# Optimization experiments

Measured on AMD Instinct MI355X. Metric: run time of the kernel, lower is better.

## Reference

```python
import jax, jax.numpy as jnp
import numpy as np

N = 50000      # nodes
E = 800000     # edges
F = 128        # node feature dim (= output_size, residual)
H = 128        # hidden_size

def _uniform_fan_avg(key, shape):
    # VarianceScaling(scale=1.0, mode='fan_avg', distribution='uniform')
    fan_avg = (shape[0] + shape[1]) / 2.0
    limit = np.sqrt(3.0 / fan_avg)
    return jax.random.uniform(key, shape, jnp.float32, -limit, limit)

def setup_inputs() -> dict:
    key = jax.random.key(0)
    ks = jax.random.split(key, 16)
    h = jax.random.normal(ks[0], (N, F), jnp.float32)
    pos = jax.random.normal(ks[1], (N, 3), jnp.float32)
    senders = jax.random.randint(ks[2], (E,), 0, N, jnp.int32)
    receivers = jax.random.randint(ks[3], (E,), 0, N, jnp.int32)
    # edge_mlp: Linear(2F+1 -> H) silu, Linear(H -> H) silu (activate_final=True)
    eW1 = _uniform_fan_avg(ks[4], (2 * F + 1, H)); eb1 = jnp.zeros((H,), jnp.float32)
    eW2 = _uniform_fan_avg(ks[5], (H, H)); eb2 = jnp.zeros((H,), jnp.float32)
    # node_mlp: Linear(F+H -> H) silu, Linear(H -> F) (no final act)
    nW1 = _uniform_fan_avg(ks[6], (F + H, H)); nb1 = jnp.zeros((H,), jnp.float32)
    nW2 = _uniform_fan_avg(ks[7], (H, F)); nb2 = jnp.zeros((F,), jnp.float32)
    # pos_correction_mlp: Linear(H -> H) silu, Linear(H -> 1, no bias, UniformScaling(dt))
    pW1 = _uniform_fan_avg(ks[8], (H, H)); pb1 = jnp.zeros((H,), jnp.float32)
    dt = 0.001
    pW2 = jax.random.uniform(ks[9], (H, 1), jnp.float32, -dt, dt) * np.sqrt(3.0)
    return {"h": h, "pos": pos, "senders": senders, "receivers": receivers,
            "eW1": eW1, "eb1": eb1, "eW2": eW2, "eb2": eb2,
            "nW1": nW1, "nb1": nb1, "nW2": nW2, "nb2": nb2,
            "pW1": pW1, "pb1": pb1, "pW2": pW2}

def reference(h, pos, senders, receivers,
              eW1, eb1, eW2, eb2,
              nW1, nb1, nW2, nb2,
              pW1, pb1, pW2):
    n = h.shape[0]
    # _coord2radial (normalize=False)
    coord_diff = pos[senders] - pos[receivers]            # [E,3]
    radial = jnp.sum(coord_diff ** 2, axis=1, keepdims=True)  # [E,1]
    # edge update (_message): concat(h[senders], h[receivers], radial) -> edge_mlp
    msg_in = jnp.concatenate([h[senders], h[receivers], radial], axis=-1)  # [E,2F+1]
    msg = jax.nn.silu(msg_in @ eW1 + eb1)
    msg = jax.nn.silu(msg @ eW2 + eb2)                    # [E,H]
    # node update (_update): aggregate messages at receivers, node_mlp, residual
    agg = jax.ops.segment_sum(msg, receivers, num_segments=n)  # [N,H]
    x = jnp.concatenate([h, agg], axis=-1)                # [N,F+H]
    x = jax.nn.silu(x @ nW1 + nb1)
    x = x @ nW2 + nb2                                     # [N,F]
    h_new = h + x                                         # residual
    # position update (_pos_update)
    pc = jax.nn.silu(msg @ pW1 + pb1) @ pW2               # [E,1]
    trans = jnp.clip(coord_diff * pc, -100, 100)          # [E,3]
    pos_new = pos + jax.ops.segment_sum(trans, senders, num_segments=n)
    return h_new, pos_new
```

## Files before the change

kernel.cpp:

```cpp
#include <hip/hip_runtime.h>
#include <hip/hip_bf16.h>

#define NNODES 50000
#define NEDGES 800000
#define EB 1024
#define SCAN_BLOCKS 196
#define TRN_BLOCKS 448

typedef short bf16x8 __attribute__((ext_vector_type(8)));
typedef float f32x4 __attribute__((ext_vector_type(4)));
typedef unsigned short u16;
typedef unsigned int u32;

__device__ __forceinline__ u16 f2bf(float f) {
    __hip_bfloat16 b = __float2bfloat16(f);
    return *reinterpret_cast<u16*>(&b);
}
__device__ __forceinline__ float bf2f(u16 v) {
    u32 u = ((u32)v) << 16;
    return __uint_as_float(u);
}
__device__ __forceinline__ u32 pack2(float a, float b) {
    __hip_bfloat162 t = __float22bfloat162_rn(float2{a, b});
    return *reinterpret_cast<u32*>(&t);
}
__device__ __forceinline__ float fast_silu(float x) {
    float e = __builtin_amdgcn_exp2f(-1.442695040888963f * x);
    return x * __builtin_amdgcn_rcpf(1.0f + e);
}
__device__ __forceinline__ bf16x8 ld8(const u16* p) {
    return *(const bf16x8*)p;
}
__device__ __forceinline__ f32x4 mfma16(bf16x8 a, bf16x8 b, f32x4 c) {
    return __builtin_amdgcn_mfma_f32_16x16x32_bf16(a, b, c, 0, 0, 0);
}
__device__ __forceinline__ void bar_lds() {
    asm volatile("s_waitcnt lgkmcnt(0)\n\ts_barrier" ::: "memory");
}

__global__ void prep_kernel(const float* __restrict__ eW1, const float* __restrict__ eW2,
                            const float* __restrict__ pW1, const float* __restrict__ nW1,
                            const float* __restrict__ nW2,
                            u16* __restrict__ eW1T, u16* __restrict__ eW2T,
                            u16* __restrict__ pW1T, u16* __restrict__ nW1T,
                            u16* __restrict__ nW2T,
                            const int* __restrict__ rcv, int* __restrict__ counts) {
    int b = blockIdx.x;
    if (b < TRN_BLOCKS) {
        int i = b * 256 + threadIdx.x;
        const float* src; u16* dst; int K;
        if (i < 32768)      { src = eW1; dst = eW1T; K = 256; }
        else if (i < 49152) { src = eW2; dst = eW2T; K = 128; i -= 32768; }
        else if (i < 65536) { src = pW1; dst = pW1T; K = 128; i -= 49152; }
        else if (i < 98304) { src = nW1; dst = nW1T; K = 256; i -= 65536; }
        else                { src = nW2; dst = nW2T; K = 128; i -= 98304; }
        int n = i / K, k = i - n * K;
        dst[i] = f2bf(src[k * 128 + n]);
    } else {
        int e = (b - TRN_BLOCKS) * 256 + threadIdx.x;
        if (e < NEDGES) atomicAdd(&counts[rcv[e]], 1);
    }
}

__global__ __launch_bounds__(256) void gemm_p(
    const float* __restrict__ h, const u16* __restrict__ eW1T,
    const u16* __restrict__ nW1T, const float* __restrict__ eb1,
    u16* __restrict__ P)
{
    const int tid  = threadIdx.x;
    const int w    = tid >> 6;
    const int lane = tid & 63;
    const int m    = lane & 15;
    const int quad = lane >> 4;
    const int ksub = quad * 8;

    bf16x8 bw[4][6];
    float bias[6];
    #pragma unroll
    for (int cc = 0; cc < 6; cc++) {
        int C = 96 * w + 16 * cc + m;
        const u16* bp;
        if (C < 128)      { bp = eW1T + C * 256;               bias[cc] = 0.5f * eb1[C]; }
        else if (C < 256) { bp = eW1T + (C - 128) * 256 + 128; bias[cc] = 0.5f * eb1[C - 128]; }
        else              { bp = nW1T + (C - 256) * 256;       bias[cc] = 0.f; }
        #pragma unroll
        for (int t = 0; t < 4; t++) bw[t][cc] = ld8(bp + t * 32 + ksub);
    }
    const int base = blockIdx.x * 64;
    #pragma unroll
    for (int mt = 0; mt < 4; mt++) {
        int nm = base + mt * 16 + m;
        if (nm >= NNODES) nm = NNODES - 1;
        bf16x8 afr[4];
        #pragma unroll
        for (int t = 0; t < 4; t++) {
            const float* ap = h + (size_t)nm * 128 + t * 32 + ksub;
            f32x4 lo = *(const f32x4*)ap;
            f32x4 hi = *(const f32x4*)(ap + 4);
            #pragma unroll
            for (int j = 0; j < 4; j++) {
                afr[t][j]     = (short)f2bf(lo[j]);
                afr[t][4 + j] = (short)f2bf(hi[j]);
            }
        }
        f32x4 acc[6];
        #pragma unroll
        for (int cc = 0; cc < 6; cc++) acc[cc] = (f32x4){0,0,0,0};
        #pragma unroll
        for (int t = 0; t < 4; t++)
            #pragma unroll
            for (int cc = 0; cc < 6; cc++)
                acc[cc] = mfma16(afr[t], bw[t][cc], acc[cc]);
        #pragma unroll
        for (int cc = 0; cc < 6; cc++) {
            int C = 96 * w + 16 * cc + m;
            #pragma unroll
            for (int r = 0; r < 4; r++) {
                int nr = base + mt * 16 + quad * 4 + r;
                if (nr < NNODES) P[(size_t)nr * 384 + C] = f2bf(acc[cc][r] + bias[cc]);
            }
        }
    }
}

__global__ void scan1(const int* __restrict__ counts, int* __restrict__ excl,
                      int* __restrict__ blkSum) {
    __shared__ int tmp[256];
    int tx = threadIdx.x;
    int i = blockIdx.x * 256 + tx;
    int v = (i < NNODES) ? counts[i] : 0;
    tmp[tx] = v;
    __syncthreads();
    for (int off = 1; off < 256; off <<= 1) {
        int t = (tx >= off) ? tmp[tx - off] : 0;
        __syncthreads();
        tmp[tx] += t;
        __syncthreads();
    }
    if (i < NNODES) excl[i] = tmp[tx] - v;
    if (tx == 255) blkSum[blockIdx.x] = tmp[255];
}
__global__ void scan2(const int* __restrict__ blkSum, int* __restrict__ blkOff) {
    __shared__ int tmp[256];
    int tx = threadIdx.x;
    int v = (tx < SCAN_BLOCKS) ? blkSum[tx] : 0;
    tmp[tx] = v;
    __syncthreads();
    for (int off = 1; off < 256; off <<= 1) {
        int t = (tx >= off) ? tmp[tx - off] : 0;
        __syncthreads();
        tmp[tx] += t;
        __syncthreads();
    }
    if (tx < SCAN_BLOCKS) blkOff[tx] = tmp[tx] - v;
}
__global__ void scan3(const int* __restrict__ excl, const int* __restrict__ blkOff,
                      int* __restrict__ cursor) {
    int i = blockIdx.x * 256 + threadIdx.x;
    if (i < NNODES) cursor[i] = excl[i] + blkOff[blockIdx.x];
}
__global__ void scatter_kernel(const int* __restrict__ rcv, int* __restrict__ cursor,
                               int* __restrict__ perm) {
    int e = blockIdx.x * 256 + threadIdx.x;
    if (e < NEDGES) {
        int p = atomicAdd(&cursor[rcv[e]], 1);
        perm[p] = e;
    }
}

struct __align__(16) EdgeLds {
    u16   m1[64 * 136];
    u16   msg[64 * 136];
    float diff[64][4];
    float pcpart[4][64];
    float wlast[128];
    int   sndloc[64];
    int   rcvloc[64];
    unsigned long long bmap;
};

__global__ __launch_bounds__(256, 4) void edge_kernel(
    const u16* __restrict__ P, const float* __restrict__ pos,
    const int* __restrict__ snd, const int* __restrict__ rcv,
    const int* __restrict__ perm,
    const float* __restrict__ eW1last,
    const u16* __restrict__ eW2T, const float* __restrict__ eb2,
    const u16* __restrict__ pW1T, const float* __restrict__ pb1,
    const float* __restrict__ pW2,
    float* __restrict__ agg, float* __restrict__ posacc)
{
    __shared__ EdgeLds S;
    const int tid  = threadIdx.x;
    const int w    = tid >> 6;
    const int lane = tid & 63;
    const int m    = lane & 15;
    const int quad = lane >> 4;
    const int ksub = quad * 8;

    bf16x8 bw2[4][2], bp1[4][2];
    float b2v[2], pb1v[2], pw2v[2];
    #pragma unroll
    for (int cc = 0; cc < 2; cc++) {
        int col = (2 * w + cc) * 16 + m;
        #pragma unroll
        for (int t = 0; t < 4; t++) {
            bw2[t][cc] = ld8(eW2T + col * 128 + t * 32 + ksub);
            bp1[t][cc] = ld8(pW1T + col * 128 + t * 32 + ksub);
        }
        b2v[cc]  = eb2[col];
        pb1v[cc] = pb1[col];
        pw2v[cc] = pW2[col];
    }
    if (tid < 128) S.wlast[tid] = eW1last[tid];

    const int stride = gridDim.x * 64;

    int s_n, r_n;
    float ps_n[3], pr_n[3];
    bf16x8 pa_n[4], pb_n[4];
    {
        int eg = perm[blockIdx.x * 64 + lane];
        s_n = snd[eg]; r_n = rcv[eg];
        #pragma unroll
        for (int c = 0; c < 3; c++) { ps_n[c] = pos[s_n * 3 + c]; pr_n[c] = pos[r_n * 3 + c]; }
        #pragma unroll
        for (int t = 0; t < 4; t++) {
            pa_n[t] = ld8(P + (size_t)s_n * 384 + w * 32 + t * 8);
            pb_n[t] = ld8(P + (size_t)r_n * 384 + 128 + w * 32 + t * 8);
        }
    }

    for (int base = blockIdx.x * 64; base < NEDGES; base += stride) {
        int nbase = base + stride;
        int pfb = (nbase < NEDGES) ? nbase : base;

        bar_lds();
        const int s = s_n, r = r_n;
        const float d0 = ps_n[0] - pr_n[0];
        const float d1 = ps_n[1] - pr_n[1];
        const float d2 = ps_n[2] - pr_n[2];
        const float rad = d0 * d0 + d1 * d1 + d2 * d2;
        bf16x8 pa[4], pb[4];
        #pragma unroll
        for (int t = 0; t < 4; t++) { pa[t] = pa_n[t]; pb[t] = pb_n[t]; }

        int eg_n = perm[pfb + lane];

        if (tid < 64) {
            S.sndloc[tid] = s; S.rcvloc[tid] = r;
            S.diff[tid][0] = d0; S.diff[tid][1] = d1; S.diff[tid][2] = d2;
            int pv = __shfl_up(r, 1);
            unsigned long long bm = __ballot(lane > 0 && r != pv);
            if (tid == 0) S.bmap = bm;
        }

        {
            const int sw = lane >> 3;
            #pragma unroll
            for (int k = 0; k < 4; k++) {
                bf16x8 va = pa[k];
                bf16x8 vb = pb[k];
                u32 pk[4];
                #pragma unroll
                for (int jj = 0; jj < 4; jj++) {
                    int col = w * 32 + k * 8 + jj * 2;
                    float2 wl = *(const float2*)&S.wlast[col];
                    float v0 = bf2f((u16)va[jj * 2])     + bf2f((u16)vb[jj * 2])     + rad * wl.x;
                    float v1 = bf2f((u16)va[jj * 2 + 1]) + bf2f((u16)vb[jj * 2 + 1]) + rad * wl.y;
                    pk[jj] = pack2(fast_silu(v0), fast_silu(v1));
                }
                int chunk = (w * 4 + k) ^ sw;
                *(uint4*)&S.m1[lane * 136 + chunk * 8] =
                    make_uint4(pk[0], pk[1], pk[2], pk[3]);
            }
        }

        s_n = snd[eg_n]; r_n = rcv[eg_n];

        bar_lds();
        #pragma unroll
        for (int mt = 0; mt < 4; mt++) {
            const int rs = mt * 2 + (m >> 3);
            const int row = mt * 16 + m;
            f32x4 acc0 = (f32x4){0,0,0,0}, acc1 = (f32x4){0,0,0,0};
            #pragma unroll
            for (int t = 0; t < 4; t++) {
                bf16x8 a = *(const bf16x8*)&S.m1[row * 136 + ((t * 4 + quad) ^ rs) * 8];
                acc0 = mfma16(a, bw2[t][0], acc0);
                acc1 = mfma16(a, bw2[t][1], acc1);
            }
            #pragma unroll
            for (int cc = 0; cc < 2; cc++) {
                f32x4 acc = cc ? acc1 : acc0;
                int col = (2 * w + cc) * 16 + m;
                #pragma unroll
                for (int rr = 0; rr < 4; rr++) {
                    int orow = mt * 16 + quad * 4 + rr;
                    S.msg[orow * 136 + col] = f2bf(fast_silu(acc[rr] + b2v[cc]));
                }
            }
        }

        #pragma unroll
        for (int c = 0; c < 3; c++) { ps_n[c] = pos[s_n * 3 + c]; pr_n[c] = pos[r_n * 3 + c]; }
        #pragma unroll
        for (int t = 0; t < 4; t++) {
            pa_n[t] = ld8(P + (size_t)s_n * 384 + w * 32 + t * 8);
            pb_n[t] = ld8(P + (size_t)r_n * 384 + 128 + w * 32 + t * 8);
        }

        bar_lds();
        #pragma unroll
        for (int mt = 0; mt < 4; mt++) {
            f32x4 acc0 = (f32x4){0,0,0,0}, acc1 = (f32x4){0,0,0,0};
            #pragma unroll
            for (int t = 0; t < 4; t++) {
                bf16x8 a = *(const bf16x8*)&S.msg[(mt * 16 + m) * 136 + t * 32 + ksub];
                acc0 = mfma16(a, bp1[t][0], acc0);
                acc1 = mfma16(a, bp1[t][1], acc1);
            }
            float p4[4];
            #pragma unroll
            for (int rr = 0; rr < 4; rr++)
                p4[rr] = fast_silu(acc0[rr] + pb1v[0]) * pw2v[0]
                       + fast_silu(acc1[rr] + pb1v[1]) * pw2v[1];
            #pragma unroll
            for (int mask = 1; mask < 16; mask <<= 1) {
                #pragma unroll
                for (int rr = 0; rr < 4; rr++) p4[rr] += __shfl_xor(p4[rr], mask);
            }
            if (m == 0) {
                #pragma unroll
                for (int rr = 0; rr < 4; rr++)
                    S.pcpart[w][mt * 16 + quad * 4 + rr] = p4[rr];
            }
        }
        {
            int half = tid >> 7, col = tid & 127;
            int r0 = half * 32;
            u32 bm32 = __builtin_amdgcn_readfirstlane((u32)(S.bmap >> r0)) & ~1u;
            float a = 0.f;
            int cur = S.rcvloc[r0];
            int rr = r0;
            const int end0 = r0 + 32;
            while (true) {
                int nb = bm32 ? (r0 + __builtin_ctz(bm32)) : end0;
                for (; rr < nb; ++rr) a += bf2f(S.msg[rr * 136 + col]);
                atomicAdd(&agg[(size_t)cur * 128 + col], a);
                if (nb == end0) break;
                a = 0.f;
                cur = S.rcvloc[nb];
                bm32 &= bm32 - 1;
            }
        }
        bar_lds();
        if (tid < 192) {
            int ee = tid / 3, c = tid - ee * 3;
            float pc = S.pcpart[0][ee] + S.pcpart[1][ee] + S.pcpart[2][ee] + S.pcpart[3][ee];
            float tr = S.diff[ee][c] * pc;
            tr = fminf(fmaxf(tr, -100.f), 100.f);
            atomicAdd(&posacc[S.sndloc[ee] * 3 + c], tr);
        }
    }
}

__global__ __launch_bounds__(256, 4) void node_kernel(
    const u16* __restrict__ P, const float* __restrict__ h,
    const float* __restrict__ agg,
    const u16* __restrict__ nW1T, const float* __restrict__ nb1,
    const u16* __restrict__ nW2T, const float* __restrict__ nb2,
    const float* __restrict__ pos, const float* __restrict__ posacc,
    float* __restrict__ out)
{
    __shared__ alignas(16) u16 m1[64 * 136];
    const int tid  = threadIdx.x;
    const int w    = tid >> 6;
    const int lane = tid & 63;
    const int m    = lane & 15;
    const int quad = lane >> 4;
    const int ksub = quad * 8;

    bf16x8 bw1[4][2], bw2[4][2];
    float b1v[2], b2v[2];
    #pragma unroll
    for (int cc = 0; cc < 2; cc++) {
        int col = (2 * w + cc) * 16 + m;
        #pragma unroll
        for (int t = 0; t < 4; t++) {
            bw1[t][cc] = ld8(nW1T + col * 256 + 128 + t * 32 + ksub);
            bw2[t][cc] = ld8(nW2T + col * 128 + t * 32 + ksub);
        }
        b1v[cc] = nb1[col];
        b2v[cc] = nb2[col];
    }
    const int base = blockIdx.x * 64;
    #pragma unroll
    for (int mt = 0; mt < 4; mt++) {
        int nm = base + mt * 16 + m;
        if (nm >= NNODES) nm = NNODES - 1;
        f32x4 acc0 = (f32x4){0,0,0,0}, acc1 = (f32x4){0,0,0,0};
        #pragma unroll
        for (int t = 0; t < 4; t++) {
            const float* ap = agg + (size_t)nm * 128 + t * 32 + ksub;
            f32x4 lo = *(const f32x4*)ap;
            f32x4 hi = *(const f32x4*)(ap + 4);
            bf16x8 a;
            #pragma unroll
            for (int j = 0; j < 4; j++) {
                a[j]     = (short)f2bf(lo[j]);
                a[4 + j] = (short)f2bf(hi[j]);
            }
            acc0 = mfma16(a, bw1[t][0], acc0);
            acc1 = mfma16(a, bw1[t][1], acc1);
        }
        #pragma unroll
        for (int cc = 0; cc < 2; cc++) {
            f32x4 acc = cc ? acc1 : acc0;
            int col = (2 * w + cc) * 16 + m;
            #pragma unroll
            for (int rr = 0; rr < 4; rr++) {
                int row = mt * 16 + quad * 4 + rr;
                int nrc = base + row; if (nrc >= NNODES) nrc = NNODES - 1;
                float v = acc[rr] + bf2f(P[(size_t)nrc * 384 + 256 + col]) + b1v[cc];
                m1[row * 136 + col] = f2bf(fast_silu(v));
            }
        }
    }
    __syncthreads();
    #pragma unroll
    for (int mt = 0; mt < 4; mt++) {
        f32x4 acc0 = (f32x4){0,0,0,0}, acc1 = (f32x4){0,0,0,0};
        #pragma unroll
        for (int t = 0; t < 4; t++) {
            bf16x8 a = *(const bf16x8*)&m1[(mt * 16 + m) * 136 + t * 32 + ksub];
            acc0 = mfma16(a, bw2[t][0], acc0);
            acc1 = mfma16(a, bw2[t][1], acc1);
        }
        #pragma unroll
        for (int cc = 0; cc < 2; cc++) {
            f32x4 acc = cc ? acc1 : acc0;
            int col = (2 * w + cc) * 16 + m;
            #pragma unroll
            for (int rr = 0; rr < 4; rr++) {
                int nr = base + mt * 16 + quad * 4 + rr;
                if (nr < NNODES)
                    out[(size_t)nr * 128 + col] = acc[rr] + b2v[cc] + h[(size_t)nr * 128 + col];
            }
        }
    }
    if (tid < 192) {
        int i = blockIdx.x * 192 + tid;
        if (i < NNODES * 3) out[NNODES * 128 + i] = pos[i] + posacc[i];
    }
}

extern "C" void kernel_launch(void* const* d_in, const int* in_sizes, int n_in,
                              void* d_out, int out_size, void* d_ws, size_t ws_size,
                              hipStream_t stream) {
    (void)in_sizes; (void)n_in; (void)out_size; (void)ws_size;
    const float* h   = (const float*)d_in[0];
    const float* pos = (const float*)d_in[1];
    const int*   snd = (const int*)d_in[2];
    const int*   rcv = (const int*)d_in[3];
    const float* eW1 = (const float*)d_in[4];
    const float* eb1 = (const float*)d_in[5];
    const float* eW2 = (const float*)d_in[6];
    const float* eb2 = (const float*)d_in[7];
    const float* nW1 = (const float*)d_in[8];
    const float* nb1 = (const float*)d_in[9];
    const float* nW2 = (const float*)d_in[10];
    const float* nb2 = (const float*)d_in[11];
    const float* pW1 = (const float*)d_in[12];
    const float* pb1 = (const float*)d_in[13];
    const float* pW2 = (const float*)d_in[14];
    float* out = (float*)d_out;

    float* agg    = (float*)d_ws;
    float* posacc = agg + (size_t)NNODES * 128;
    u16* P    = (u16*)(posacc + (size_t)NNODES * 3);
    u16* eW1T = P + (size_t)NNODES * 384;
    u16* eW2T = eW1T + 128 * 256;
    u16* pW1T = eW2T + 128 * 128;
    u16* nW1T = pW1T + 128 * 128;
    u16* nW2T = nW1T + 128 * 256;
    int* counts = (int*)(nW2T + 128 * 128);
    int* excl   = counts + 50048;
    int* blkSum = excl + 50048;
    int* blkOff = blkSum + 256;
    int* cursor = blkOff + 256;
    int* perm   = cursor + 50048;

    hipMemsetAsync(agg, 0, (size_t)NNODES * 131 * sizeof(float), stream);
    hipMemsetAsync(counts, 0, 50048 * sizeof(int), stream);

    prep_kernel<<<TRN_BLOCKS + (NEDGES + 255) / 256, 256, 0, stream>>>(
        eW1, eW2, pW1, nW1, nW2, eW1T, eW2T, pW1T, nW1T, nW2T, rcv, counts);

    gemm_p<<<(NNODES + 63) / 64, 256, 0, stream>>>(h, eW1T, nW1T, eb1, P);

    scan1<<<SCAN_BLOCKS, 256, 0, stream>>>(counts, excl, blkSum);
    scan2<<<1, 256, 0, stream>>>(blkSum, blkOff);
    scan3<<<SCAN_BLOCKS, 256, 0, stream>>>(excl, blkOff, cursor);
    scatter_kernel<<<(NEDGES + 255) / 256, 256, 0, stream>>>(rcv, cursor, perm);

    edge_kernel<<<EB, 256, 0, stream>>>(
        P, pos, snd, rcv, perm,
        eW1 + 256 * 128,
        eW2T, eb2, pW1T, pb1, pW2,
        agg, posacc);

    node_kernel<<<(NNODES + 63) / 64, 256, 0, stream>>>(
        P, h, agg, nW1T, nb1, nW2T, nb2, pos, posacc, out);
}
```

Baseline: 553.0 us.

## Assign edge tiles per XCD contiguously and drop register prefetch of gathered rows

Edge tiles are now split into eight contiguous ranges, one per XCD, chosen from blockIdx&7. Each XCD's blocks stride through their own range, so receiver-sorted tiles that share node rows hit the same L2. The software prefetch of pos and projected-feature rows into registers for the next tile is removed, and those gathers now happen at use time. This cuts register pressure, which may help occupancy, but exposes gather latency and assumes the grid holds 8*128 blocks.

Result: faster. 454.9 us (-17.7%).

```diff
diff --git a/kernel.cpp b/kernel.cpp
--- a/kernel.cpp
+++ b/kernel.cpp
@@ -213,39 +213,31 @@
     }
     if (tid < 128) S.wlast[tid] = eW1last[tid];
 
-    const int stride = gridDim.x * 64;
-
-    int s_n, r_n;
-    float ps_n[3], pr_n[3];
-    bf16x8 pa_n[4], pb_n[4];
-    {
-        int eg = perm[blockIdx.x * 64 + lane];
-        s_n = snd[eg]; r_n = rcv[eg];
-        #pragma unroll
-        for (int c = 0; c < 3; c++) { ps_n[c] = pos[s_n * 3 + c]; pr_n[c] = pos[r_n * 3 + c]; }
-        #pragma unroll
-        for (int t = 0; t < 4; t++) {
-            pa_n[t] = ld8(P + (size_t)s_n * 384 + w * 32 + t * 8);
-            pb_n[t] = ld8(P + (size_t)r_n * 384 + 128 + w * 32 + t * 8);
-        }
-    }
-
-    for (int base = blockIdx.x * 64; base < NEDGES; base += stride) {
-        int nbase = base + stride;
-        int pfb = (nbase < NEDGES) ? nbase : base;
+    const int NT  = NEDGES / 64;
+    const int xcd = blockIdx.x & 7;
+    const int ib  = blockIdx.x >> 3;
+    const int per = (NT + 7) / 8;
+    const int t0  = xcd * per;
+    const int t1  = (t0 + per < NT) ? t0 + per : NT;
+
+    int eg_n = 0, s_n = 0, r_n = 0;
+    if (t0 + ib < t1) {
+        eg_n = perm[(t0 + ib) * 64 + lane];
+        s_n = snd[eg_n]; r_n = rcv[eg_n];
+    }
+
+    for (int t = t0 + ib; t < t1; t += 128) {
+        const int s = s_n, r = r_n;
+        const int tn = t + 128;
+        const int tp = (tn < t1) ? tn : t;
+        int eg2 = perm[tp * 64 + lane];
+
+        float d0 = pos[s * 3 + 0] - pos[r * 3 + 0];
+        float d1 = pos[s * 3 + 1] - pos[r * 3 + 1];
+        float d2 = pos[s * 3 + 2] - pos[r * 3 + 2];
+        float rad = d0 * d0 + d1 * d1 + d2 * d2;
 
         bar_lds();
-        const int s = s_n, r = r_n;
-        const float d0 = ps_n[0] - pr_n[0];
-        const float d1 = ps_n[1] - pr_n[1];
-        const float d2 = ps_n[2] - pr_n[2];
-        const float rad = d0 * d0 + d1 * d1 + d2 * d2;
-        bf16x8 pa[4], pb[4];
-        #pragma unroll
-        for (int t = 0; t < 4; t++) { pa[t] = pa_n[t]; pb[t] = pb_n[t]; }
-
-        int eg_n = perm[pfb + lane];
-
         if (tid < 64) {
             S.sndloc[tid] = s; S.rcvloc[tid] = r;
             S.diff[tid][0] = d0; S.diff[tid][1] = d1; S.diff[tid][2] = d2;
@@ -253,13 +245,14 @@
             unsigned long long bm = __ballot(lane > 0 && r != pv);
             if (tid == 0) S.bmap = bm;
         }
-
         {
             const int sw = lane >> 3;
+            const u16* pa = P + (size_t)s * 384 + w * 32;
+            const u16* pb = P + (size_t)r * 384 + 128 + w * 32;
             #pragma unroll
             for (int k = 0; k < 4; k++) {
-                bf16x8 va = pa[k];
-                bf16x8 vb = pb[k];
+                bf16x8 va = ld8(pa + k * 8);
+                bf16x8 vb = ld8(pb + k * 8);
                 u32 pk[4];
                 #pragma unroll
                 for (int jj = 0; jj < 4; jj++) {
@@ -274,8 +267,7 @@
                     make_uint4(pk[0], pk[1], pk[2], pk[3]);
             }
         }
-
-        s_n = snd[eg_n]; r_n = rcv[eg_n];
+        s_n = snd[eg2]; r_n = rcv[eg2]; eg_n = eg2;
 
         bar_lds();
         #pragma unroll
@@ -284,10 +276,10 @@
             const int row = mt * 16 + m;
             f32x4 acc0 = (f32x4){0,0,0,0}, acc1 = (f32x4){0,0,0,0};
             #pragma unroll
-            for (int t = 0; t < 4; t++) {
-                bf16x8 a = *(const bf16x8*)&S.m1[row * 136 + ((t * 4 + quad) ^ rs) * 8];
-                acc0 = mfma16(a, bw2[t][0], acc0);
-                acc1 = mfma16(a, bw2[t][1], acc1);
+            for (int t4 = 0; t4 < 4; t4++) {
+                bf16x8 a = *(const bf16x8*)&S.m1[row * 136 + ((t4 * 4 + quad) ^ rs) * 8];
+                acc0 = mfma16(a, bw2[t4][0], acc0);
+                acc1 = mfma16(a, bw2[t4][1], acc1);
             }
             #pragma unroll
             for (int cc = 0; cc < 2; cc++) {
@@ -300,24 +292,15 @@
                 }
             }
         }
-
-        #pragma unroll
-        for (int c = 0; c < 3; c++) { ps_n[c] = pos[s_n * 3 + c]; pr_n[c] = pos[r_n * 3 + c]; }
-        #pragma unroll
-        for (int t = 0; t < 4; t++) {
-            pa_n[t] = ld8(P + (size_t)s_n * 384 + w * 32 + t * 8);
-            pb_n[t] = ld8(P + (size_t)r_n * 384 + 128 + w * 32 + t * 8);
-        }
-
         bar_lds();
         #pragma unroll
         for (int mt = 0; mt < 4; mt++) {
             f32x4 acc0 = (f32x4){0,0,0,0}, acc1 = (f32x4){0,0,0,0};
             #pragma unroll
-            for (int t = 0; t < 4; t++) {
-                bf16x8 a = *(const bf16x8*)&S.msg[(mt * 16 + m) * 136 + t * 32 + ksub];
-                acc0 = mfma16(a, bp1[t][0], acc0);
-                acc1 = mfma16(a, bp1[t][1], acc1);
+            for (int t4 = 0; t4 < 4; t4++) {
+                bf16x8 a = *(const bf16x8*)&S.msg[(mt * 16 + m) * 136 + t4 * 32 + ksub];
+                acc0 = mfma16(a, bp1[t4][0], acc0);
+                acc1 = mfma16(a, bp1[t4][1], acc1);
             }
             float p4[4];
             #pragma unroll
```
